# Kernel tuning notes

Measured on AMD Instinct MI355X. Metric: run time of the kernel, lower is better.

## Reference

```python
import jax, jax.numpy as jnp
import numpy as np
import math

N_EMBD = 1024
N_HEAD = 16
HEAD_DIM = N_EMBD // N_HEAD
B, T = 2, 2048
LORA_RANK = 16      # 8-bit setting
LORA_SCALE = 32.0 / 16.0  # alpha / rank
QMIN, QMAX = 0.0, 255.0   # 8-bit asymmetric


def round_ste(x):
    return x + jax.lax.stop_gradient(jnp.round(x) - x)


def fake_quant(x, scale, zero_point):
    # LearnableFakeQuantize, asymmetric 8-bit, straight-through round
    q = jnp.clip(round_ste(x / scale + zero_point), QMIN, QMAX)
    return (q - zero_point) * scale


def lora_linear(x, w, b, la, lb):
    # base linear + LoRA path (dropout disabled / eval)
    return x @ w + b + LORA_SCALE * ((x @ la) @ lb)


def setup_inputs() -> dict:
    key = jax.random.key(0)
    ks = jax.random.split(key, 10)
    std = 0.02
    hidden_states = jax.random.normal(ks[0], (B, T, N_EMBD), dtype=jnp.float32)
    w_attn = jax.random.normal(ks[1], (N_EMBD, 3 * N_EMBD), dtype=jnp.float32) * std
    b_attn = jnp.zeros((3 * N_EMBD,), dtype=jnp.float32)
    la_attn = jax.random.normal(ks[2], (N_EMBD, LORA_RANK), dtype=jnp.float32) * std
    lb_attn = jnp.zeros((LORA_RANK, 3 * N_EMBD), dtype=jnp.float32)
    w_proj = jax.random.normal(ks[3], (N_EMBD, N_EMBD), dtype=jnp.float32) * std
    b_proj = jnp.zeros((N_EMBD,), dtype=jnp.float32)
    la_proj = jax.random.normal(ks[4], (N_EMBD, LORA_RANK), dtype=jnp.float32) * std
    lb_proj = jnp.zeros((LORA_RANK, N_EMBD), dtype=jnp.float32)
    kv_scale = jnp.asarray(0.05, dtype=jnp.float32)
    kv_zero_point = jnp.asarray(128.0, dtype=jnp.float32)
    return {
        'hidden_states': hidden_states,
        'w_attn': w_attn, 'b_attn': b_attn, 'la_attn': la_attn, 'lb_attn': lb_attn,
        'w_proj': w_proj, 'b_proj': b_proj, 'la_proj': la_proj, 'lb_proj': lb_proj,
        'kv_scale': kv_scale, 'kv_zero_point': kv_zero_point,
    }


def reference(hidden_states, w_attn, b_attn, la_attn, lb_attn,
              w_proj, b_proj, la_proj, lb_proj, kv_scale, kv_zero_point):
    Bn, Tn, C = hidden_states.shape
    qkv = lora_linear(hidden_states, w_attn, b_attn, la_attn, lb_attn)
    q, k, v = jnp.split(qkv, 3, axis=2)
    # [B, T, C] -> [B, H, T, D]
    def to_heads(x):
        return x.reshape(Bn, Tn, N_HEAD, HEAD_DIM).transpose(0, 2, 1, 3)
    q, k, v = to_heads(q), to_heads(k), to_heads(v)
    k = fake_quant(k, kv_scale, kv_zero_point)
    v = fake_quant(v, kv_scale, kv_zero_point)
    scores = jnp.einsum('bhqd,bhkd->bhqk', q, k) / math.sqrt(HEAD_DIM)
    causal = jnp.tril(jnp.ones((Tn, Tn), dtype=bool))
    scores = jnp.where(causal, scores, -jnp.inf)
    attn = jax.nn.softmax(scores, axis=-1)
    out = jnp.einsum('bhqk,bhkd->bhqd', attn, v)
    out = out.transpose(0, 2, 1, 3).reshape(Bn, Tn, C)
    return lora_linear(out, w_proj, b_proj, la_proj, lb_proj)
```

## Files before the change

### kernel.cpp

```cpp
#include <hip/hip_runtime.h>
#include <hip/hip_bf16.h>
#include <math.h>

#define N_EMBD   1024
#define N_HEAD   16
#define HEAD_DIM 64
#define BATCH    2
#define TSEQ     2048
#define RANK     16
#define LORA_SCALE 2.0f
#define M_TOTAL  (BATCH * TSEQ)
#define C3       (3 * N_EMBD)

typedef unsigned short ushort_t;
typedef __attribute__((ext_vector_type(8))) short bf16x8;
typedef __attribute__((ext_vector_type(4))) float f32x4;

__device__ __forceinline__ float fake_quant(float x, float scale, float zp) {
    float q = rintf(x / scale + zp);
    q = fminf(fmaxf(q, 0.0f), 255.0f);
    return (q - zp) * scale;
}

__device__ __forceinline__ ushort_t bf16bits(float f) {
    union { __hip_bfloat16 h; ushort_t u; } c;
    c.h = __float2bfloat16(f);
    return c.u;
}

__device__ __forceinline__ float bfraw2f(ushort_t u) {
    union { unsigned int i; float f; } c; c.i = ((unsigned int)u) << 16; return c.f;
}

__global__ void cvt_split_kernel(const float* __restrict__ in,
                                 __hip_bfloat16* __restrict__ hi,
                                 __hip_bfloat16* __restrict__ lo, int n4) {
    int i = blockIdx.x * 256 + threadIdx.x;
    if (i >= n4) return;
    float4 v = ((const float4*)in)[i];
    float vs[4] = {v.x, v.y, v.z, v.w};
    #pragma unroll
    for (int k = 0; k < 4; ++k) {
        __hip_bfloat16 h = __float2bfloat16(vs[k]);
        hi[i * 4 + k] = h;
        lo[i * 4 + k] = __float2bfloat16(vs[k] - __bfloat162float(h));
    }
}

__global__ void transpose_split_kernel(const float* __restrict__ in,
                                       __hip_bfloat16* __restrict__ hiT,
                                       __hip_bfloat16* __restrict__ loT,
                                       int R, int C) {
    __shared__ float tl[32][33];
    const int c0 = blockIdx.x * 32, r0 = blockIdx.y * 32;
    const int tx = threadIdx.x & 31, ty = threadIdx.x >> 5;
    for (int i = ty; i < 32; i += 8)
        tl[i][tx] = in[(size_t)(r0 + i) * C + c0 + tx];
    __syncthreads();
    for (int i = ty; i < 32; i += 8) {
        float v = tl[tx][i];
        __hip_bfloat16 h = __float2bfloat16(v);
        size_t o = (size_t)(c0 + i) * R + r0 + tx;
        hiT[o] = h;
        if (loT) loT[o] = __float2bfloat16(v - __bfloat162float(h));
    }
}

__global__ void vtrans_kernel(const ushort_t* __restrict__ Vb,
                              ushort_t* __restrict__ Vt) {
    __shared__ ushort_t tl[64][68];
    const int bh = blockIdx.x & 31, tt = blockIdx.x >> 5;
    const int tid = threadIdx.x;
    {
        const int t = tid >> 2, d0 = (tid & 3) * 16;
        const uint4 u = *(const uint4*)(Vb + ((size_t)bh * TSEQ + tt * 64 + t) * 64 + d0);
        *(uint4*)&tl[t][d0] = u;
        *(uint4*)&tl[t][d0 + 8] = *(const uint4*)(Vb + ((size_t)bh * TSEQ + tt * 64 + t) * 64 + d0 + 8);
    }
    __syncthreads();
    const int d = tid >> 2, t0 = (tid & 3) * 16;
    unsigned int wbuf[8];
    #pragma unroll
    for (int j = 0; j < 8; ++j)
        wbuf[j] = (unsigned int)tl[t0 + 2 * j][d] | ((unsigned int)tl[t0 + 2 * j + 1][d] << 16);
    ushort_t* dst = Vt + ((size_t)bh * 64 + d) * TSEQ + tt * 64 + t0;
    *(uint4*)dst       = make_uint4(wbuf[0], wbuf[1], wbuf[2], wbuf[3]);
    *(uint4*)(dst + 8) = make_uint4(wbuf[4], wbuf[5], wbuf[6], wbuf[7]);
}

__global__ void lora_t_part_kernel(const float* __restrict__ x,
                                   const float* __restrict__ la,
                                   float* __restrict__ tpart, int K) {
    __shared__ float Xs[16][64];
    const int tid = threadIdx.x;
    const int ty = tid >> 4, tx = tid & 15;
    const int row0 = blockIdx.x * 16;
    const int kbase = blockIdx.y * 256;
    float acc = 0.0f;
    for (int k0 = kbase; k0 < kbase + 256; k0 += 64) {
        int rr = tid >> 4, kk = (tid & 15) * 4;
        float4 v = *(const float4*)(x + (size_t)(row0 + rr) * K + k0 + kk);
        Xs[rr][kk] = v.x; Xs[rr][kk + 1] = v.y; Xs[rr][kk + 2] = v.z; Xs[rr][kk + 3] = v.w;
        __syncthreads();
        for (int k = 0; k < 64; ++k)
            acc += Xs[ty][k] * la[(size_t)(k0 + k) * RANK + tx];
        __syncthreads();
    }
    tpart[((size_t)blockIdx.y * M_TOTAL + row0 + ty) * RANK + tx] = acc;
}

__global__ void lora_t_part_bf16_kernel(const ushort_t* __restrict__ x,
                                        const float* __restrict__ la,
                                        float* __restrict__ tpart, int K) {
    __shared__ float Xs[16][64];
    const int tid = threadIdx.x;
    const int ty = tid >> 4, tx = tid & 15;
    const int row0 = blockIdx.x * 16;
    const int kbase = blockIdx.y * 256;
    float acc = 0.0f;
    for (int k0 = kbase; k0 < kbase + 256; k0 += 64) {
        int rr = tid >> 4, kk = (tid & 15) * 4;
        const ushort4 u = *(const ushort4*)(x + (size_t)(row0 + rr) * K + k0 + kk);
        Xs[rr][kk] = bfraw2f(u.x); Xs[rr][kk + 1] = bfraw2f(u.y);
        Xs[rr][kk + 2] = bfraw2f(u.z); Xs[rr][kk + 3] = bfraw2f(u.w);
        __syncthreads();
        for (int k = 0; k < 64; ++k)
            acc += Xs[ty][k] * la[(size_t)(k0 + k) * RANK + tx];
        __syncthreads();
    }
    tpart[((size_t)blockIdx.y * M_TOTAL + row0 + ty) * RANK + tx] = acc;
}

__device__ __forceinline__ int sw_off(int r, int c) {
    return ((r >> 1) << 7) + (((((r & 1) << 2) | c) ^ ((r >> 1) & 7)) << 4);
}

template <bool SPLIT>
__global__ __launch_bounds__(256, 3)
void gemm_mfma_kernel(const __hip_bfloat16* __restrict__ Ah,
                      const __hip_bfloat16* __restrict__ Al,
                      const __hip_bfloat16* __restrict__ Bh,
                      const __hip_bfloat16* __restrict__ Bl,
                      const float* __restrict__ bias,
                      const float* __restrict__ tpart,
                      const float* __restrict__ lb,
                      float* __restrict__ Cf,
                      ushort_t* __restrict__ Qb,
                      ushort_t* __restrict__ Kb,
                      ushort_t* __restrict__ Vb,
                      const float* __restrict__ sp,
                      const float* __restrict__ zp,
                      int M, int N, int K, int split_col0, int out_mode) {
    constexpr int TILE = 128 * 32;
    __shared__ __hip_bfloat16 As[(SPLIT ? 2 : 1) * TILE];
    __shared__ __hip_bfloat16 Bs[(SPLIT ? 2 : 1) * TILE];
    __shared__ float Ts[128 * 16];
    __shared__ float Ls[16 * 128];

    const int tid = threadIdx.x;
    const int lane = tid & 63, w = tid >> 6;

    int bcol, brow, phase;
    {
        const int NC = gridDim.x, NR = gridDim.y;
        const int lid = blockIdx.y * NC + blockIdx.x;
        const int xcd = lid & 7, s = lid >> 3;
        const int cw = NC >> 1, rh = NR >> 2;
        const int cg = xcd & 1, rg = xcd >> 1;
        bcol = cg * cw + (s % cw);
        brow = rg * rh + (s / cw);
        phase = (lid * 7) & 31;
    }
    const int row0 = brow * 128, col0 = bcol * 128;
    const int wr = (w >> 1) * 64, wc = (w & 1) * 64;
    const bool do_split = SPLIT && (col0 >= split_col0);

    const int s_lc = (lane & 7) ^ ((lane >> 3) & 7);
    const int s_rb = 2 * (lane >> 3) + (s_lc >> 2);
    const int s_c8 = (s_lc & 3) * 8;

    float qsc = 0.f, qzp = 0.f;
    if (out_mode == 1) { qsc = sp[0]; qzp = zp[0]; }

    f32x4 acc[4][4];
    #pragma unroll
    for (int i = 0; i < 4; ++i)
        #pragma unroll
        for (int j = 0; j < 4; ++j)
            acc[i][j] = (f32x4){0.f, 0.f, 0.f, 0.f};

    const int arow = wr + (lane & 15);
    const int chunk = lane >> 4;

    const int KI = K >> 5;
    for (int kk = 0; kk < KI; ++kk) {
        const int k0 = (((kk + phase) & (KI - 1)) << 5);
        #pragma unroll
        for (int qq = 0; qq < 2; ++qq) {
            const int q = 2 * w + qq;
            const int r = 16 * q + s_rb;
            const __hip_bfloat16* gA = Ah + (size_t)(row0 + r) * K + k0 + s_c8;
            __builtin_amdgcn_global_load_lds(
                (const __attribute__((address_space(1))) void*)gA,
                (__attribute__((address_space(3))) void*)(As + q * 512), 16, 0, 0);
            const __hip_bfloat16* gB = Bh + (size_t)(col0 + r) * K + k0 + s_c8;
            __builtin_amdgcn_global_load_lds(
                (const __attribute__((address_space(1))) void*)gB,
                (__attribute__((address_space(3))) void*)(Bs + q * 512), 16, 0, 0);
            if (do_split) {
                const __hip_bfloat16* gAl = Al + (size_t)(row0 + r) * K + k0 + s_c8;
                __builtin_amdgcn_global_load_lds(
                    (const __attribute__((address_space(1))) void*)gAl,
                    (__attribute__((address_space(3))) void*)(As + TILE + q * 512), 16, 0, 0);
                const __hip_bfloat16* gBl = Bl + (size_t)(col0 + r) * K + k0 + s_c8;
                __builtin_amdgcn_global_load_lds(
                    (const __attribute__((address_space(1))) void*)gBl,
                    (__attribute__((address_space(3))) void*)(Bs + TILE + q * 512), 16, 0, 0);
            }
        }
        __syncthreads();

        const char* ab = (const char*)As;
        const char* bb = (const char*)Bs;
        bf16x8 a_h[4], b_h[4], a_l[4], b_l[4];
        #pragma unroll
        for (int mi = 0; mi < 4; ++mi) {
            int off = sw_off(arow + mi * 16, chunk);
            a_h[mi] = *(const bf16x8*)(ab + off);
            if (do_split) a_l[mi] = *(const bf16x8*)(ab + 2 * TILE + off);
        }
        #pragma unroll
        for (int nj = 0; nj < 4; ++nj) {
            int off = sw_off(wc + nj * 16 + (lane & 15), chunk);
            b_h[nj] = *(const bf16x8*)(bb + off);
            if (do_split) b_l[nj] = *(const bf16x8*)(bb + 2 * TILE + off);
        }
        #pragma unroll
        for (int mi = 0; mi < 4; ++mi)
            #pragma unroll
            for (int nj = 0; nj < 4; ++nj) {
                acc[mi][nj] = __builtin_amdgcn_mfma_f32_16x16x32_bf16(a_h[mi], b_h[nj], acc[mi][nj], 0, 0, 0);
                if (do_split) {
                    acc[mi][nj] = __builtin_amdgcn_mfma_f32_16x16x32_bf16(a_h[mi], b_l[nj], acc[mi][nj], 0, 0, 0);
                    acc[mi][nj] = __builtin_amdgcn_mfma_f32_16x16x32_bf16(a_l[mi], b_h[nj], acc[mi][nj], 0, 0, 0);
                }
            }
        __syncthreads();
    }

    {
        int r = tid >> 1, j0 = (tid & 1) * 8;
        float4 t0 = {0, 0, 0, 0}, t1 = {0, 0, 0, 0};
        #pragma unroll
        for (int c = 0; c < 4; ++c) {
            const float* src = tpart + ((size_t)c * M_TOTAL + row0 + r) * RANK + j0;
            float4 s0 = *(const float4*)src;
            float4 s1 = *(const float4*)(src + 4);
            t0.x += s0.x; t0.y += s0.y; t0.z += s0.z; t0.w += s0.w;
            t1.x += s1.x; t1.y += s1.y; t1.z += s1.z; t1.w += s1.w;
        }
        *(float4*)(Ts + r * 16 + j0)     = t0;
        *(float4*)(Ts + r * 16 + j0 + 4) = t1;
        int rr = tid >> 4, c0 = (tid & 15) * 8;
        const float4* lsrc = (const float4*)(lb + (size_t)rr * N + col0 + c0);
        float4* ldst = (float4*)(Ls + rr * 128 + c0);
        ldst[0] = lsrc[0]; ldst[1] = lsrc[1];
    }
    __syncthreads();
    #pragma unroll
    for (int mi = 0; mi < 4; ++mi)
        #pragma unroll
        for (int nj = 0; nj < 4; ++nj) {
            const int coll = wc + nj * 16 + (lane & 15);
            const float bv = bias[col0 + coll];
            #pragma unroll
            for (int rg = 0; rg < 4; ++rg) {
                const int rowl = wr + mi * 16 + (lane >> 4) * 4 + rg;
                float lsum = 0.f;
                #pragma unroll
                for (int rr = 0; rr < 16; ++rr)
                    lsum += Ts[rowl * 16 + rr] * Ls[rr * 128 + coll];
                const float val = acc[mi][nj][rg] + bv + LORA_SCALE * lsum;
                if (out_mode == 0) {
                    Cf[(size_t)(row0 + rowl) * N + col0 + coll] = val;
                } else {
                    const int R = row0 + rowl;
                    const int b = R >> 11, t = R & 2047;
                    const int CN = col0 + coll;
                    const int sec = CN >> 10, head = (CN >> 6) & 15, d = CN & 63;
                    const size_t off = (((size_t)(b * 16 + head)) * TSEQ + t) * 64 + d;
                    if (sec == 0)      Qb[off] = bf16bits(val * 0.125f);
                    else if (sec == 1) Kb[off] = bf16bits(fake_quant(val, qsc, qzp));
                    else               Vb[off] = bf16bits(fake_quant(val, qsc, qzp));
                }
            }
        }
}

__global__ __launch_bounds__(256)
void mfma_attn_kernel(const ushort_t* __restrict__ Qb,
                      const ushort_t* __restrict__ Kq,
                      const ushort_t* __restrict__ Vtq,
                      ushort_t* __restrict__ outb) {
    const int bx = blockIdx.x;
    const int bh = bx & 31;
    const int qt = 31 - (bx >> 5);
    const int b = bh >> 4, h = bh & 15;
    const int tid = threadIdx.x;
    const int lane = tid & 63, w = tid >> 6;
    const int m16 = lane & 15, qc = lane >> 4;
    const int m7 = m16 & 7;

    __shared__ ushort_t Qs[4096];
    __shared__ ushort_t Ks[4096];
    __shared__ ushort_t Vs[4096];
    __shared__ ushort_t Ps[4096];

    const int s_g = (lane & 7) ^ ((lane >> 3) & 7);
    const int s_r = lane >> 3;

    const ushort_t* Qg = Qb + (size_t)bh * TSEQ * 64;
    const ushort_t* Kg = Kq + (size_t)bh * TSEQ * 64;
    const ushort_t* Vg = Vtq + (size_t)bh * 64 * TSEQ;

    #pragma unroll
    for (int pp = 0; pp < 2; ++pp) {
        const int p = 2 * w + pp;
        const ushort_t* gq = Qg + ((size_t)(qt * 64 + 8 * p + s_r)) * 64 + s_g * 8;
        __builtin_amdgcn_global_load_lds(
            (const __attribute__((address_space(1))) void*)gq,
            (__attribute__((address_space(3))) void*)(Qs + p * 512), 16, 0, 0);
    }
    __syncthreads();

    bf16x8 a_q[2];
    {
        const int row = 16 * w + m16;
        #pragma unroll
        for (int c = 0; c < 2; ++c) {
            const int g = qc + 4 * c;
            a_q[c] = *(const bf16x8*)((const char*)Qs + row * 128 + ((g ^ m7) << 4));
        }
    }

    float m_st[4], l_st[4];
    f32x4 o_acc[4];
    #pragma unroll
    for (int r = 0; r < 4; ++r) { m_st[r] = -INFINITY; l_st[r] = 0.0f; }
    #pragma unroll
    for (int dj = 0; dj < 4; ++dj) o_acc[dj] = (f32x4){0.f, 0.f, 0.f, 0.f};

    for (int kt = 0; kt <= qt; ++kt) {
        __syncthreads();
        #pragma unroll
        for (int pp = 0; pp < 2; ++pp) {
            const int p = 2 * w + pp;
            const ushort_t* gk = Kg + ((size_t)(kt * 64 + 8 * p + s_r)) * 64 + s_g * 8;
            __builtin_amdgcn_global_load_lds(
                (const __attribute__((address_space(1))) void*)gk,
                (__attribute__((address_space(3))) void*)(Ks + p * 512), 16, 0, 0);
            const ushort_t* gv = Vg + ((size_t)(8 * p + s_r)) * TSEQ + kt * 64 + s_g * 8;
            __builtin_amdgcn_global_load_lds(
                (const __attribute__((address_space(1))) void*)gv,
                (__attribute__((address_space(3))) void*)(Vs + p * 512), 16, 0, 0);
        }
        __syncthreads();

        const bool diag = (kt == qt);
        const int nj_hi = diag ? (w + 1) : 4;

        f32x4 s[4];
        #pragma unroll
        for (int nj = 0; nj < 4; ++nj) s[nj] = (f32x4){0.f, 0.f, 0.f, 0.f};
        #pragma unroll
        for (int c = 0; c < 2; ++c) {
            #pragma unroll
            for (int nj = 0; nj < 4; ++nj) {
                if (nj < nj_hi) {
                    const int row = 16 * nj + m16;
                    const int g = qc + 4 * c;
                    bf16x8 bk = *(const bf16x8*)((const char*)Ks + row * 128 + ((g ^ m7) << 4));
                    s[nj] = __builtin_amdgcn_mfma_f32_16x16x32_bf16(a_q[c], bk, s[nj], 0, 0, 0);
                }
            }
        }

        float alpha[4], p_[4][4];
        #pragma unroll
        for (int reg = 0; reg < 4; ++reg) {
            const int qrow = 16 * w + 4 * qc + reg;
            float sv[4];
            float rm = -INFINITY;
            #pragma unroll
            for (int nj = 0; nj < 4; ++nj) {
                float v = s[nj][reg];
                if (diag && (m16 + 16 * nj > qrow)) v = -INFINITY;
                sv[nj] = v;
                rm = fmaxf(rm, v);
            }
            #pragma unroll
            for (int off = 1; off < 16; off <<= 1)
                rm = fmaxf(rm, __shfl_xor(rm, off, 16));
            const float mo = m_st[reg];
            const float mn = fmaxf(mo, rm);
            const float al = __expf(mo - mn);
            float rs = 0.f;
            #pragma unroll
            for (int nj = 0; nj < 4; ++nj) {
                float pv = __expf(sv[nj] - mn);
                p_[reg][nj] = pv;
                rs += pv;
            }
            #pragma unroll
            for (int off = 1; off < 16; off <<= 1)
                rs += __shfl_xor(rs, off, 16);
            l_st[reg] = al * l_st[reg] + rs;
            m_st[reg] = mn;
            alpha[reg] = al;
        }

        #pragma unroll
        for (int reg = 0; reg < 4; ++reg) {
            const int row = 16 * w + 4 * qc + reg;
            const int r7 = row & 7;
            #pragma unroll
            for (int nj = 0; nj < 4; ++nj) {
                const int k = m16 + 16 * nj;
                Ps[row * 64 + (((k >> 3) ^ r7) << 3) + (k & 7)] = bf16bits(p_[reg][nj]);
            }
        }

        #pragma unroll
        for (int dj = 0; dj < 4; ++dj)
            #pragma unroll
            for (int reg = 0; reg < 4; ++reg)
                o_acc[dj][reg] *= alpha[reg];

        const int c_hi = diag ? (w >= 2 ? 2 : 1) : 2;
        #pragma unroll
        for (int c = 0; c < 2; ++c) {
            if (c < c_hi) {
                const int rowp = 16 * w + m16;
                const int g = qc + 4 * c;
                bf16x8 ap = *(const bf16x8*)((const char*)Ps + rowp * 128 + ((g ^ m7) << 4));
                #pragma unroll
                for (int dj = 0; dj < 4; ++dj) {
                    const int rowv = 16 * dj + m16;
                    bf16x8 bv = *(const bf16x8*)((const char*)Vs + rowv * 128 + ((g ^ m7) << 4));
                    o_acc[dj] = __builtin_amdgcn_mfma_f32_16x16x32_bf16(ap, bv, o_acc[dj], 0, 0, 0);
                }
            }
        }
    }

    #pragma unroll
    for (int reg = 0; reg < 4; ++reg) {
        const float inv = 1.0f / l_st[reg];
        const int q = qt * 64 + 16 * w + 4 * qc + reg;
        #pragma unroll
        for (int dj = 0; dj < 4; ++dj) {
            const int d = m16 + 16 * dj;
            outb[((size_t)b * TSEQ + q) * N_EMBD + h * 64 + d] = bf16bits(o_acc[dj][reg] * inv);
        }
    }
}

extern "C" void kernel_launch(void* const* d_in, const int* in_sizes, int n_in,
                              void* d_out, int out_size, void* d_ws, size_t ws_size,
                              hipStream_t stream) {
    const float* x        = (const float*)d_in[0];
    const float* w_attn   = (const float*)d_in[1];
    const float* b_attn   = (const float*)d_in[2];
    const float* la_attn  = (const float*)d_in[3];
    const float* lb_attn  = (const float*)d_in[4];
    const float* w_proj   = (const float*)d_in[5];
    const float* b_proj   = (const float*)d_in[6];
    const float* la_proj  = (const float*)d_in[7];
    const float* lb_proj  = (const float*)d_in[8];
    const float* kv_scale = (const float*)d_in[9];
    const float* kv_zp    = (const float*)d_in[10];
    float* out = (float*)d_out;

    char* ws = (char*)d_ws;
    float* t_attn_p       = (float*)ws;          ws += (size_t)4 * M_TOTAL * RANK * 4;
    float* t_proj_p       = (float*)ws;          ws += (size_t)4 * M_TOTAL * RANK * 4;
    ushort_t* aob         = (ushort_t*)ws;       ws += (size_t)M_TOTAL * N_EMBD * 2;
    __hip_bfloat16* x_hi  = (__hip_bfloat16*)ws; ws += (size_t)M_TOTAL * N_EMBD * 2;
    __hip_bfloat16* x_lo  = (__hip_bfloat16*)ws; ws += (size_t)M_TOTAL * N_EMBD * 2;
    __hip_bfloat16* wqT_h = (__hip_bfloat16*)ws; ws += (size_t)C3 * N_EMBD * 2;
    __hip_bfloat16* wqT_l = (__hip_bfloat16*)ws; ws += (size_t)C3 * N_EMBD * 2;
    __hip_bfloat16* wpT   = (__hip_bfloat16*)ws; ws += (size_t)N_EMBD * N_EMBD * 2;
    ushort_t* Qb          = (ushort_t*)ws;       ws += (size_t)32 * TSEQ * 64 * 2;
    ushort_t* Kb          = (ushort_t*)ws;       ws += (size_t)32 * TSEQ * 64 * 2;
    ushort_t* Vb          = (ushort_t*)ws;       ws += (size_t)32 * TSEQ * 64 * 2;
    ushort_t* Vtq         = (ushort_t*)ws;       ws += (size_t)32 * 64 * TSEQ * 2;

    cvt_split_kernel<<<dim3(M_TOTAL * N_EMBD / 4 / 256), 256, 0, stream>>>(
        x, x_hi, x_lo, M_TOTAL * N_EMBD / 4);
    transpose_split_kernel<<<dim3(C3 / 32, N_EMBD / 32), 256, 0, stream>>>(
        w_attn, wqT_h, wqT_l, N_EMBD, C3);
    transpose_split_kernel<<<dim3(N_EMBD / 32, N_EMBD / 32), 256, 0, stream>>>(
        w_proj, wpT, nullptr, N_EMBD, N_EMBD);
    lora_t_part_kernel<<<dim3(M_TOTAL / 16, 4), 256, 0, stream>>>(x, la_attn, t_attn_p, N_EMBD);

    gemm_mfma_kernel<true><<<dim3(C3 / 128, M_TOTAL / 128), 256, 0, stream>>>(
        x_hi, x_lo, wqT_h, wqT_l, b_attn, t_attn_p, lb_attn,
        nullptr, Qb, Kb, Vb, kv_scale, kv_zp,
        M_TOTAL, C3, N_EMBD, 2 * N_EMBD, 1);

    vtrans_kernel<<<dim3(32 * (TSEQ / 64)), 256, 0, stream>>>(Vb, Vtq);

    mfma_attn_kernel<<<dim3(32 * 32), 256, 0, stream>>>(Qb, Kb, Vtq, aob);

    lora_t_part_bf16_kernel<<<dim3(M_TOTAL / 16, 4), 256, 0, stream>>>(aob, la_proj, t_proj_p, N_EMBD);

    gemm_mfma_kernel<false><<<dim3(N_EMBD / 128, M_TOTAL / 128), 256, 0, stream>>>(
        (const __hip_bfloat16*)aob, nullptr, wpT, nullptr, b_proj, t_proj_p, lb_proj,
        out, nullptr, nullptr, nullptr, nullptr, nullptr,
        M_TOTAL, N_EMBD, N_EMBD, 1 << 30, 0);
}
```

Measured before the change: 348.6 us.

## Fold split-bf16 V projection into a concatenated K=3072 GEMM with unified tiles

The hi/lo split-precision products for the V columns are now expressed as one longer-K GEMM. Activations are stored as [hi|lo|hi] along K and the V weights as [hi|hi|lo], so a single bf16 MFMA per step covers all three cross terms. This removes the doubled LDS tiles and the conditional extra loads and MFMAs per step, which shrinks shared memory and lets occupancy rise from 3 to 4 blocks. The grid becomes a 1D launch in which V blocks run 96 K-steps and Q/K blocks run 32, so per-block work is imbalanced. The prep kernels also write an extra 3x-wide activation buffer.

```diff
diff --git a/kernel.cpp b/kernel.cpp
--- a/kernel.cpp
+++ b/kernel.cpp
@@ -11,6 +11,7 @@
 #define LORA_SCALE 2.0f
 #define M_TOTAL  (BATCH * TSEQ)
 #define C3       (3 * N_EMBD)
+#define KCAT     3072
 
 typedef unsigned short ushort_t;
 typedef __attribute__((ext_vector_type(8))) short bf16x8;
@@ -32,25 +33,28 @@
     union { unsigned int i; float f; } c; c.i = ((unsigned int)u) << 16; return c.f;
 }
 
-__global__ void cvt_split_kernel(const float* __restrict__ in,
-                                 __hip_bfloat16* __restrict__ hi,
-                                 __hip_bfloat16* __restrict__ lo, int n4) {
+__global__ void cvt_cat_kernel(const float* __restrict__ in,
+                               ushort_t* __restrict__ xcat, int n4) {
     int i = blockIdx.x * 256 + threadIdx.x;
     if (i >= n4) return;
     float4 v = ((const float4*)in)[i];
-    float vs[4] = {v.x, v.y, v.z, v.w};
-    #pragma unroll
-    for (int k = 0; k < 4; ++k) {
-        __hip_bfloat16 h = __float2bfloat16(vs[k]);
-        hi[i * 4 + k] = h;
-        lo[i * 4 + k] = __float2bfloat16(vs[k] - __bfloat162float(h));
-    }
-}
-
-__global__ void transpose_split_kernel(const float* __restrict__ in,
-                                       __hip_bfloat16* __restrict__ hiT,
-                                       __hip_bfloat16* __restrict__ loT,
-                                       int R, int C) {
+    const int row = i >> 8;
+    const int c4  = (i & 255) * 4;
+    ushort4 h4, l4;
+    h4.x = bf16bits(v.x); l4.x = bf16bits(v.x - bfraw2f(h4.x));
+    h4.y = bf16bits(v.y); l4.y = bf16bits(v.y - bfraw2f(h4.y));
+    h4.z = bf16bits(v.z); l4.z = bf16bits(v.z - bfraw2f(h4.z));
+    h4.w = bf16bits(v.w); l4.w = bf16bits(v.w - bfraw2f(h4.w));
+    ushort_t* base = xcat + (size_t)row * KCAT;
+    *(ushort4*)(base + c4)        = h4;
+    *(ushort4*)(base + 1024 + c4) = l4;
+    *(ushort4*)(base + 2048 + c4) = h4;
+}
+
+__global__ void transpose_cat_kernel(const float* __restrict__ in,
+                                     ushort_t* __restrict__ hiT,
+                                     ushort_t* __restrict__ vcat,
+                                     int R, int C) {
     __shared__ float tl[32][33];
     const int c0 = blockIdx.x * 32, r0 = blockIdx.y * 32;
     const int tx = threadIdx.x & 31, ty = threadIdx.x >> 5;
@@ -59,10 +63,15 @@
     __syncthreads();
     for (int i = ty; i < 32; i += 8) {
         float v = tl[tx][i];
-        __hip_bfloat16 h = __float2bfloat16(v);
-        size_t o = (size_t)(c0 + i) * R + r0 + tx;
-        hiT[o] = h;
-        if (loT) loT[o] = __float2bfloat16(v - __bfloat162float(h));
+        ushort_t h = bf16bits(v);
+        hiT[(size_t)(c0 + i) * R + r0 + tx] = h;
+        if (vcat && (c0 + i) >= 2048) {
+            size_t o = (size_t)(c0 + i - 2048) * KCAT + r0 + tx;
+            ushort_t l = bf16bits(v - bfraw2f(h));
+            vcat[o]        = h;
+            vcat[o + 1024] = h;
+            vcat[o + 2048] = l;
+        }
     }
 }
 
@@ -135,12 +144,11 @@
     return ((r >> 1) << 7) + (((((r & 1) << 2) | c) ^ ((r >> 1) & 7)) << 4);
 }
 
-template <bool SPLIT>
-__global__ __launch_bounds__(256, 3)
-void gemm_mfma_kernel(const __hip_bfloat16* __restrict__ Ah,
-                      const __hip_bfloat16* __restrict__ Al,
-                      const __hip_bfloat16* __restrict__ Bh,
-                      const __hip_bfloat16* __restrict__ Bl,
+template <bool QKV>
+__global__ __launch_bounds__(256, 4)
+void gemm_mfma_kernel(const ushort_t* __restrict__ A,
+                      const ushort_t* __restrict__ B,
+                      const ushort_t* __restrict__ Bv,
                       const float* __restrict__ bias,
                       const float* __restrict__ tpart,
                       const float* __restrict__ lb,
@@ -150,18 +158,37 @@
                       ushort_t* __restrict__ Vb,
                       const float* __restrict__ sp,
                       const float* __restrict__ zp,
-                      int M, int N, int K, int split_col0, int out_mode) {
+                      int M, int N, int K) {
     constexpr int TILE = 128 * 32;
-    __shared__ __hip_bfloat16 As[(SPLIT ? 2 : 1) * TILE];
-    __shared__ __hip_bfloat16 Bs[(SPLIT ? 2 : 1) * TILE];
+    __shared__ ushort_t As[TILE];
+    __shared__ ushort_t Bs[TILE];
     __shared__ float Ts[128 * 16];
     __shared__ float Ls[16 * 128];
 
     const int tid = threadIdx.x;
     const int lane = tid & 63, w = tid >> 6;
 
-    int bcol, brow, phase;
-    {
+    int bcol, brow, phase, KI, sA, sB;
+    const ushort_t* Bbase;
+    if (QKV) {
+        const int lid = blockIdx.x;
+        if (lid < 256) {
+            const int xcd = lid & 7, s = lid >> 3;
+            bcol = 16 + (xcd & 3) * 2 + (s & 1);
+            brow = (xcd >> 2) * 16 + (s >> 1);
+            KI = 96;
+        } else {
+            const int q = lid - 256;
+            const int xcd = q & 7, s = q >> 3;
+            bcol = (xcd & 3) * 4 + (s & 3);
+            brow = (xcd >> 2) * 16 + (s >> 2);
+            KI = 32;
+        }
+        phase = (lid * 7 + (lid >> 8) * 11) & 31;
+        sA = KCAT;
+        if (KI == 96) { Bbase = Bv + (size_t)(bcol * 128 - 2048) * KCAT; sB = KCAT; }
+        else          { Bbase = B + (size_t)(bcol * 128) * 1024; sB = 1024; }
+    } else {
         const int NC = gridDim.x, NR = gridDim.y;
         const int lid = blockIdx.y * NC + blockIdx.x;
         const int xcd = lid & 7, s = lid >> 3;
@@ -170,17 +197,18 @@
         bcol = cg * cw + (s % cw);
         brow = rg * rh + (s / cw);
         phase = (lid * 7) & 31;
+        KI = K >> 5; sA = K; sB = K;
+        Bbase = B + (size_t)(bcol * 128) * K;
     }
     const int row0 = brow * 128, col0 = bcol * 128;
     const int wr = (w >> 1) * 64, wc = (w & 1) * 64;
-    const bool do_split = SPLIT && (col0 >= split_col0);
 
     const int s_lc = (lane & 7) ^ ((lane >> 3) & 7);
     const int s_rb = 2 * (lane >> 3) + (s_lc >> 2);
     const int s_c8 = (s_lc & 3) * 8;
 
     float qsc = 0.f, qzp = 0.f;
-    if (out_mode == 1) { qsc = sp[0]; qzp = zp[0]; }
+    if (QKV) { qsc = sp[0]; qzp = zp[0]; }
 
     f32x4 acc[4][4];
     #pragma unroll
@@ -192,59 +220,38 @@
     const int arow = wr + (lane & 15);
     const int chunk = lane >> 4;
 
-    const int KI = K >> 5;
     for (int kk = 0; kk < KI; ++kk) {
-        const int k0 = (((kk + phase) & (KI - 1)) << 5);
+        int kidx = kk + phase; if (kidx >= KI) kidx -= KI;
+        const int k0 = kidx << 5;
         #pragma unroll
         for (int qq = 0; qq < 2; ++qq) {
             const int q = 2 * w + qq;
             const int r = 16 * q + s_rb;
-            const __hip_bfloat16* gA = Ah + (size_t)(row0 + r) * K + k0 + s_c8;
+            const ushort_t* gA = A + (size_t)(row0 + r) * sA + k0 + s_c8;
             __builtin_amdgcn_global_load_lds(
                 (const __attribute__((address_space(1))) void*)gA,
                 (__attribute__((address_space(3))) void*)(As + q * 512), 16, 0, 0);
-            const __hip_bfloat16* gB = Bh + (size_t)(col0 + r) * K + k0 + s_c8;
+            const ushort_t* gB = Bbase + (size_t)r * sB + k0 + s_c8;
             __builtin_amdgcn_global_load_lds(
                 (const __attribute__((address_space(1))) void*)gB,
                 (__attribute__((address_space(3))) void*)(Bs + q * 512), 16, 0, 0);
-            if (do_split) {
-                const __hip_bfloat16* gAl = Al + (size_t)(row0 + r) * K + k0 + s_c8;
-                __builtin_amdgcn_global_load_lds(
-                    (const __attribute__((address_space(1))) void*)gAl,
-                    (__attribute__((address_space(3))) void*)(As + TILE + q * 512), 16, 0, 0);
-                const __hip_bfloat16* gBl = Bl + (size_t)(col0 + r) * K + k0 + s_c8;
-                __builtin_amdgcn_global_load_lds(
-                    (const __attribute__((address_space(1))) void*)gBl,
-                    (__attribute__((address_space(3))) void*)(Bs + TILE + q * 512), 16, 0, 0);
-            }
         }
         __syncthreads();
 
         const char* ab = (const char*)As;
         const char* bb = (const char*)Bs;
-        bf16x8 a_h[4], b_h[4], a_l[4], b_l[4];
-        #pragma unroll
-        for (int mi = 0; mi < 4; ++mi) {
-            int off = sw_off(arow + mi * 16, chunk);
-            a_h[mi] = *(const bf16x8*)(ab + off);
-            if (do_split) a_l[mi] = *(const bf16x8*)(ab + 2 * TILE + off);
-        }
-        #pragma unroll
-        for (int nj = 0; nj < 4; ++nj) {
-            int off = sw_off(wc + nj * 16 + (lane & 15), chunk);
-            b_h[nj] = *(const bf16x8*)(bb + off);
-            if (do_split) b_l[nj] = *(const bf16x8*)(bb + 2 * TILE + off);
-        }
+        bf16x8 a_h[4], b_h[4];
         #pragma unroll
         for (int mi = 0; mi < 4; ++mi)
-            #pragma unroll
-            for (int nj = 0; nj < 4; ++nj) {
+            a_h[mi] = *(const bf16x8*)(ab + sw_off(arow + mi * 16, chunk));
+        #pragma unroll
+        for (int nj = 0; nj < 4; ++nj)
+            b_h[nj] = *(const bf16x8*)(bb + sw_off(wc + nj * 16 + (lane & 15), chunk));
+        #pragma unroll
+        for (int mi = 0; mi < 4; ++mi)
+            #pragma unroll
+            for (int nj = 0; nj < 4; ++nj)
                 acc[mi][nj] = __builtin_amdgcn_mfma_f32_16x16x32_bf16(a_h[mi], b_h[nj], acc[mi][nj], 0, 0, 0);
-                if (do_split) {
-                    acc[mi][nj] = __builtin_amdgcn_mfma_f32_16x16x32_bf16(a_h[mi], b_l[nj], acc[mi][nj], 0, 0, 0);
-                    acc[mi][nj] = __builtin_amdgcn_mfma_f32_16x16x32_bf16(a_l[mi], b_h[nj], acc[mi][nj], 0, 0, 0);
-                }
-            }
         __syncthreads();
     }
 
@@ -281,7 +288,7 @@
                 for (int rr = 0; rr < 16; ++rr)
                     lsum += Ts[rowl * 16 + rr] * Ls[rr * 128 + coll];
                 const float val = acc[mi][nj][rg] + bv + LORA_SCALE * lsum;
-                if (out_mode == 0) {
+                if constexpr (!QKV) {
                     Cf[(size_t)(row0 + rowl) * N + col0 + coll] = val;
                 } else {
                     const int R = row0 + rowl;
@@ -482,31 +489,30 @@
     float* out = (float*)d_out;
 
     char* ws = (char*)d_ws;
-    float* t_attn_p       = (float*)ws;          ws += (size_t)4 * M_TOTAL * RANK * 4;
-    float* t_proj_p       = (float*)ws;          ws += (size_t)4 * M_TOTAL * RANK * 4;
-    ushort_t* aob         = (ushort_t*)ws;       ws += (size_t)M_TOTAL * N_EMBD * 2;
-    __hip_bfloat16* x_hi  = (__hip_bfloat16*)ws; ws += (size_t)M_TOTAL * N_EMBD * 2;
-    __hip_bfloat16* x_lo  = (__hip_bfloat16*)ws; ws += (size_t)M_TOTAL * N_EMBD * 2;
-    __hip_bfloat16* wqT_h = (__hip_bfloat16*)ws; ws += (size_t)C3 * N_EMBD * 2;
-    __hip_bfloat16* wqT_l = (__hip_bfloat16*)ws; ws += (size_t)C3 * N_EMBD * 2;
-    __hip_bfloat16* wpT   = (__hip_bfloat16*)ws; ws += (size_t)N_EMBD * N_EMBD * 2;
-    ushort_t* Qb          = (ushort_t*)ws;       ws += (size_t)32 * TSEQ * 64 * 2;
-    ushort_t* Kb          = (ushort_t*)ws;       ws += (size_t)32 * TSEQ * 64 * 2;
-    ushort_t* Vb          = (ushort_t*)ws;       ws += (size_t)32 * TSEQ * 64 * 2;
-    ushort_t* Vtq         = (ushort_t*)ws;       ws += (size_t)32 * 64 * TSEQ * 2;
-
-    cvt_split_kernel<<<dim3(M_TOTAL * N_EMBD / 4 / 256), 256, 0, stream>>>(
-        x, x_hi, x_lo, M_TOTAL * N_EMBD / 4);
-    transpose_split_kernel<<<dim3(C3 / 32, N_EMBD / 32), 256, 0, stream>>>(
-        w_attn, wqT_h, wqT_l, N_EMBD, C3);
-    transpose_split_kernel<<<dim3(N_EMBD / 32, N_EMBD / 32), 256, 0, stream>>>(
+    float* t_attn_p   = (float*)ws;     ws += (size_t)4 * M_TOTAL * RANK * 4;
+    float* t_proj_p   = (float*)ws;     ws += (size_t)4 * M_TOTAL * RANK * 4;
+    ushort_t* aob     = (ushort_t*)ws;  ws += (size_t)M_TOTAL * N_EMBD * 2;
+    ushort_t* x_cat   = (ushort_t*)ws;  ws += (size_t)M_TOTAL * KCAT * 2;
+    ushort_t* wqT_h   = (ushort_t*)ws;  ws += (size_t)C3 * N_EMBD * 2;
+    ushort_t* wVcat   = (ushort_t*)ws;  ws += (size_t)N_EMBD * KCAT * 2;
+    ushort_t* wpT     = (ushort_t*)ws;  ws += (size_t)N_EMBD * N_EMBD * 2;
+    ushort_t* Qb      = (ushort_t*)ws;  ws += (size_t)32 * TSEQ * 64 * 2;
+    ushort_t* Kb      = (ushort_t*)ws;  ws += (size_t)32 * TSEQ * 64 * 2;
+    ushort_t* Vb      = (ushort_t*)ws;  ws += (size_t)32 * TSEQ * 64 * 2;
+    ushort_t* Vtq     = (ushort_t*)ws;  ws += (size_t)32 * 64 * TSEQ * 2;
+
+    cvt_cat_kernel<<<dim3(M_TOTAL * N_EMBD / 4 / 256), 256, 0, stream>>>(
+        x, x_cat, M_TOTAL * N_EMBD / 4);
+    transpose_cat_kernel<<<dim3(C3 / 32, N_EMBD / 32), 256, 0, stream>>>(
+        w_attn, wqT_h, wVcat, N_EMBD, C3);
+    transpose_cat_kernel<<<dim3(N_EMBD / 32, N_EMBD / 32), 256, 0, stream>>>(
         w_proj, wpT, nullptr, N_EMBD, N_EMBD);
     lora_t_part_kernel<<<dim3(M_TOTAL / 16, 4), 256, 0, stream>>>(x, la_attn, t_attn_p, N_EMBD);
 
-    gemm_mfma_kernel<true><<<dim3(C3 / 128, M_TOTAL / 128), 256, 0, stream>>>(
-        x_hi, x_lo, wqT_h, wqT_l, b_attn, t_attn_p, lb_attn,
+    gemm_mfma_kernel<true><<<dim3(768), 256, 0, stream>>>(
+        x_cat, wqT_h, wVcat, b_attn, t_attn_p, lb_attn,
         nullptr, Qb, Kb, Vb, kv_scale, kv_zp,
-        M_TOTAL, C3, N_EMBD, 2 * N_EMBD, 1);
+        M_TOTAL, C3, N_EMBD);
 
     vtrans_kernel<<<dim3(32 * (TSEQ / 64)), 256, 0, stream>>>(Vb, Vtq);
 
@@ -514,8 +520,8 @@
 
     lora_t_part_bf16_kernel<<<dim3(M_TOTAL / 16, 4), 256, 0, stream>>>(aob, la_proj, t_proj_p, N_EMBD);
 
-    gemm_mfma_kernel<false><<<dim3(N_EMBD / 128, M_TOTAL / 128), 256, 0, stream>>>(
-        (const __hip_bfloat16*)aob, nullptr, wpT, nullptr, b_proj, t_proj_p, lb_proj,
+    gemm_mfma_kernel<false><<<dim3(8, 32), 256, 0, stream>>>(
+        aob, wpT, nullptr, b_proj, t_proj_p, lb_proj,
         out, nullptr, nullptr, nullptr, nullptr, nullptr,
-        M_TOTAL, N_EMBD, N_EMBD, 1 << 30, 0);
-}
+        M_TOTAL, N_EMBD, N_EMBD);
+}
```

New measurement: 524.1 us. 50.4% more time.
